# Kernel tuning notes

Measured on AMD Instinct MI355X. Metric: run time of the kernel, lower is better.

Reference implementation:

```python
import jax, jax.numpy as jnp
import numpy as np


def log_g(x):
    # log of g(x) = where(x>=0, x+0.5, sigmoid(x))
    return jnp.where(x >= 0, jnp.log(jax.nn.relu(x) + 0.5), -jax.nn.softplus(-x))


def heinsen_scan_log(log_coeffs, log_values):
    # associative scan in log space over seq dim (axis=1)
    a_star = jnp.cumsum(log_coeffs, axis=1)
    log_h0_plus_b_star = jax.lax.cumlogsumexp(log_values - a_star, axis=1)
    return jnp.exp(a_star + log_h0_plus_b_star)


def setup_inputs() -> dict:
    key = jax.random.key(0)
    k1, k2, k3 = jax.random.split(key, 3)
    B, S, D_IN, D_INNER, D_OUT = 4, 4096, 1024, 1024, 1024
    x = jax.random.normal(k1, (B, S, D_IN), dtype=jnp.float32)
    # xavier_normal for Linear(d_in, 2*d_inner): std = sqrt(2/(fan_in+fan_out))
    std_hg = float(np.sqrt(2.0 / (D_IN + 2 * D_INNER)))
    W_hg = jax.random.normal(k2, (2 * D_INNER, D_IN), dtype=jnp.float32) * std_hg
    std_out = float(np.sqrt(2.0 / (D_INNER + D_OUT)))
    W_out = jax.random.normal(k3, (D_OUT, D_INNER), dtype=jnp.float32) * std_out
    return {"x": x, "W_hg": W_hg, "W_out": W_out}


def reference(x, W_hg, W_out):
    # x: [B,S,Din]; W_hg: [2*Dinner, Din]; W_out: [Dout, Dinner]
    hg = jnp.einsum("bsd,ed->bse", x, W_hg)
    hidden, gate = jnp.split(hg, 2, axis=-1)
    log_coeffs = -jax.nn.softplus(gate)        # log(1 - z)
    log_z = -jax.nn.softplus(-gate)            # log(z)
    log_values = log_z + log_g(hidden)
    h = heinsen_scan_log(log_coeffs, log_values)  # [B,S,Dinner]
    out = jnp.einsum("bsd,od->bso", h, W_out)
    return out
```

## Files before the change

kernel.cpp:

```cpp
#include <hip/hip_runtime.h>
#include <math.h>


typedef unsigned short ushort_t;
typedef unsigned int uint_t;
typedef __attribute__((ext_vector_type(4))) float f32x4;
typedef __attribute__((ext_vector_type(8))) __bf16 bf16x8;
typedef __attribute__((ext_vector_type(8))) unsigned short u16x8;

constexpr int Bsz  = 4;
constexpr int S    = 4096;
constexpr int Din  = 1024;
constexpr int Dh   = 1024;
constexpr int M    = Bsz * S;
constexpr int NCH  = 64;
constexpr int CL   = S / NCH;

__device__ __forceinline__ unsigned short f2bf(float f) {
    unsigned int u = __float_as_uint(f);
    unsigned int r = (u + 0x7fffu + ((u >> 16) & 1u)) >> 16;
    return (unsigned short)r;
}
__device__ __forceinline__ float bf2f(unsigned short u) {
    return __uint_as_float(((unsigned int)u) << 16);
}
__device__ __forceinline__ float sigf(float x) {
    x = fminf(fmaxf(x, -30.f), 30.f);
    return 1.0f / (1.0f + __expf(-x));
}
__device__ __forceinline__ void gld_lds16(const ushort_t* g, ushort_t* l) {
    __builtin_amdgcn_global_load_lds(
        (const __attribute__((address_space(1))) void*)g,
        (__attribute__((address_space(3))) void*)l, 16, 0, 0);
}

__global__ __launch_bounds__(256) void cvt_all(
    const float* __restrict__ x, const float* __restrict__ whg,
    const float* __restrict__ wout,
    ushort_t* __restrict__ xb, ushort_t* __restrict__ whgb,
    ushort_t* __restrict__ woutb)
{
    constexpr int NX = M * Din / 8;
    constexpr int NW = 2048 * 1024 / 8;
    const int i = blockIdx.x * 256 + threadIdx.x;
    const float* src; ushort_t* dst; int k;
    if (i < NX)            { src = x;    dst = xb;    k = i; }
    else if (i < NX + NW)  { src = whg;  dst = whgb;  k = i - NX; }
    else                   { src = wout; dst = woutb; k = i - NX - NW; }
    const float4 a = ((const float4*)src)[(size_t)k * 2];
    const float4 b = ((const float4*)src)[(size_t)k * 2 + 1];
    u16x8 o;
    o[0] = f2bf(a.x); o[1] = f2bf(a.y); o[2] = f2bf(a.z); o[3] = f2bf(a.w);
    o[4] = f2bf(b.x); o[5] = f2bf(b.y); o[6] = f2bf(b.z); o[7] = f2bf(b.w);
    ((u16x8*)dst)[k] = o;
}

template<bool OUT_BF16>
__global__ __launch_bounds__(512, 2) void gemm8p(
    const ushort_t* __restrict__ A, int lda,
    const ushort_t* __restrict__ B, int ldb,
    void* __restrict__ Cout, int ldc, int K, int nbx_log2)
{
    __shared__ ushort_t lds[4][2][8192];

    const int P = K >> 5;

    const int nwg = gridDim.x;
    const int cpx = nwg >> 3;
    const int bid = blockIdx.x;
    const int swz = (bid & 7) * cpx + (bid >> 3);
    const int bx  = swz & ((1 << nbx_log2) - 1);
    const int by  = swz >> nbx_log2;
    const int bm0 = by * 256;
    const int bn0 = bx * 256;

    const int t  = threadIdx.x;
    const int w  = t >> 6;
    const int l  = t & 63;
    const int wr = w >> 2;
    const int wc = w & 3;

    const int fr = l & 15;
    const int kg = l >> 4;
    const int qp = kg ^ (((fr >> 3) & 1) << 1);
    const int a_base = wr * 4096 + fr * 32 + qp * 8;
    const int b_base = wc * 2048 + fr * 32 + qp * 8;

    const int rs = l >> 2;
    const int lq = (l & 3) ^ (((rs >> 3) & 1) << 1);
    const ushort_t* gA0 = A + (size_t)(bm0 + w * 16 + rs) * lda + lq * 8;
    const ushort_t* gA1 = gA0 + (size_t)128 * lda;
    const ushort_t* gB0 = B + (size_t)(bn0 + w * 16 + rs) * ldb + lq * 8;
    const ushort_t* gB1 = gB0 + (size_t)128 * ldb;

    f32x4 acc[8][4];
    #pragma unroll
    for (int i = 0; i < 8; ++i)
        #pragma unroll
        for (int j = 0; j < 4; ++j)
            acc[i][j] = (f32x4){0.f, 0.f, 0.f, 0.f};

    auto stageA = [&](int p) {
        const int s2 = p & 3;
        const int ko = p * 32;
        gld_lds16(gA0 + ko, &lds[s2][0][w * 512]);
        gld_lds16(gA1 + ko, &lds[s2][0][w * 512 + 4096]);
    };
    auto stageB = [&](int p) {
        const int s2 = p & 3;
        const int ko = p * 32;
        gld_lds16(gB0 + ko, &lds[s2][1][w * 512]);
        gld_lds16(gB1 + ko, &lds[s2][1][w * 512 + 4096]);
    };

    stageA(0); stageB(0); stageA(1); stageB(1);
    asm volatile("s_waitcnt vmcnt(4)" ::: "memory");
    __builtin_amdgcn_s_barrier();
    __builtin_amdgcn_sched_barrier(0);

    #pragma unroll 1
    for (int p = 0; p < P; ++p) {
        const int s = p & 3;
        const ushort_t* la = &lds[s][0][0];
        const ushort_t* lb = &lds[s][1][0];
        bf16x8 bfr[4], af0[4], af1[4];

        #pragma unroll
        for (int j = 0; j < 4; ++j)
            bfr[j] = *reinterpret_cast<const bf16x8*>(&lb[b_base + j * 512]);
        #pragma unroll
        for (int i = 0; i < 4; ++i)
            af0[i] = *reinterpret_cast<const bf16x8*>(&la[a_base + i * 512]);
        if (p + 2 < P) stageA(p + 2);
        __builtin_amdgcn_sched_barrier(0);
        __builtin_amdgcn_s_barrier();
        asm volatile("s_waitcnt lgkmcnt(0)" ::: "memory");
        __builtin_amdgcn_sched_barrier(0);
        __builtin_amdgcn_s_setprio(1);
        #pragma unroll
        for (int i = 0; i < 4; ++i)
            #pragma unroll
            for (int j = 0; j < 4; ++j)
                acc[i][j] = __builtin_amdgcn_mfma_f32_16x16x32_bf16(
                    af0[i], bfr[j], acc[i][j], 0, 0, 0);
        __builtin_amdgcn_s_setprio(0);
        __builtin_amdgcn_sched_barrier(0);
        #pragma unroll
        for (int i = 0; i < 4; ++i)
            af1[i] = *reinterpret_cast<const bf16x8*>(&la[a_base + (4 + i) * 512]);
        __builtin_amdgcn_sched_barrier(0);
        __builtin_amdgcn_s_barrier();
        __builtin_amdgcn_sched_barrier(0);

        if (p + 2 < P) stageB(p + 2);
        __builtin_amdgcn_sched_barrier(0);
        if (p + 2 < P)
            asm volatile("s_waitcnt vmcnt(4)" ::: "memory");
        else if (p + 1 < P)
            asm volatile("s_waitcnt vmcnt(0)" ::: "memory");
        __builtin_amdgcn_s_barrier();
        asm volatile("s_waitcnt lgkmcnt(0)" ::: "memory");
        __builtin_amdgcn_sched_barrier(0);
        __builtin_amdgcn_s_setprio(1);
        #pragma unroll
        for (int i = 0; i < 4; ++i)
            #pragma unroll
            for (int j = 0; j < 4; ++j)
                acc[4 + i][j] = __builtin_amdgcn_mfma_f32_16x16x32_bf16(
                    af1[i], bfr[j], acc[4 + i][j], 0, 0, 0);
        __builtin_amdgcn_s_setprio(0);
        __builtin_amdgcn_sched_barrier(0);
        __builtin_amdgcn_s_barrier();
        __builtin_amdgcn_sched_barrier(0);
    }

    #pragma unroll
    for (int i = 0; i < 8; ++i) {
        #pragma unroll
        for (int j = 0; j < 4; ++j) {
            const int col = bn0 + wc * 64 + j * 16 + fr;
            #pragma unroll
            for (int r = 0; r < 4; ++r) {
                const int row = bm0 + wr * 128 + i * 16 + kg * 4 + r;
                if (OUT_BF16)
                    ((ushort_t*)Cout)[(size_t)row * ldc + col] = f2bf(acc[i][j][r]);
                else
                    ((float*)Cout)[(size_t)row * ldc + col] = acc[i][j][r];
            }
        }
    }
}


__global__ __launch_bounds__(256) void scan_stage1(
    const ushort_t* __restrict__ hg, float* __restrict__ Abuf,
    float* __restrict__ hlbuf)
{
    const int bid   = blockIdx.x;
    const int half  = bid & 1;
    const int chunk = (bid >> 1) & (NCH - 1);
    const int b     = bid >> 7;
    const int t     = threadIdx.x;
    const int d     = half * 512 + 2 * t;
    const size_t rowbase = (size_t)(b * S + chunk * CL) * 2048 + d;

    float h0 = 0.f, h1 = 0.f, A0 = 1.f, A1 = 1.f;
    #pragma unroll 4
    for (int i = 0; i < CL; ++i) {
        const ushort_t* rp = hg + rowbase + (size_t)i * 2048;
        const uint_t hp = *(const uint_t*)rp;
        const uint_t gp = *(const uint_t*)(rp + 1024);
        const float hid0 = bf2f((ushort_t)hp), hid1 = bf2f((ushort_t)(hp >> 16));
        const float g0 = bf2f((ushort_t)gp),  g1 = bf2f((ushort_t)(gp >> 16));
        const float c0 = sigf(-g0), z0 = 1.f - c0;
        const float c1 = sigf(-g1), z1 = 1.f - c1;
        const float gv0 = (hid0 >= 0.f) ? (hid0 + 0.5f) : sigf(hid0);
        const float gv1 = (hid1 >= 0.f) ? (hid1 + 0.5f) : sigf(hid1);
        h0 = fmaf(c0, h0, z0 * gv0);  A0 *= c0;
        h1 = fmaf(c1, h1, z1 * gv1);  A1 *= c1;
    }
    const size_t pb = (size_t)(b * NCH + chunk) * 1024 + d;
    *(float2*)&Abuf[pb]  = make_float2(A0, A1);
    *(float2*)&hlbuf[pb] = make_float2(h0, h1);
}

__global__ __launch_bounds__(256) void scan_stage2(
    const float* __restrict__ Abuf, const float* __restrict__ hlbuf,
    float* __restrict__ Hs)
{
    const int g = blockIdx.x * 256 + threadIdx.x;
    const int d = g & (Dh - 1);
    const int b = g >> 10;
    float h = 0.0f;
    for (int ch = 0; ch < NCH; ++ch) {
        const size_t o = (size_t)(b * NCH + ch) * Dh + d;
        Hs[o] = h;
        h = fmaf(Abuf[o], h, hlbuf[o]);
    }
}

__global__ __launch_bounds__(256) void scan_stage3(
    const ushort_t* __restrict__ hg, const float* __restrict__ Hs,
    ushort_t* __restrict__ hout)
{
    const int bid   = blockIdx.x;
    const int half  = bid & 1;
    const int chunk = (bid >> 1) & (NCH - 1);
    const int b     = bid >> 7;
    const int t     = threadIdx.x;
    const int d     = half * 512 + 2 * t;
    const size_t rowbase = (size_t)(b * S + chunk * CL) * 2048 + d;
    const size_t hb      = (size_t)(b * S + chunk * CL) * 1024 + d;

    const float2 hs = *(const float2*)&Hs[(size_t)(b * NCH + chunk) * 1024 + d];
    float h0 = hs.x, h1 = hs.y;
    #pragma unroll 4
    for (int i = 0; i < CL; ++i) {
        const ushort_t* rp = hg + rowbase + (size_t)i * 2048;
        const uint_t hp = *(const uint_t*)rp;
        const uint_t gp = *(const uint_t*)(rp + 1024);
        const float hid0 = bf2f((ushort_t)hp), hid1 = bf2f((ushort_t)(hp >> 16));
        const float g0 = bf2f((ushort_t)gp),  g1 = bf2f((ushort_t)(gp >> 16));
        const float c0 = sigf(-g0), z0 = 1.f - c0;
        const float c1 = sigf(-g1), z1 = 1.f - c1;
        const float gv0 = (hid0 >= 0.f) ? (hid0 + 0.5f) : sigf(hid0);
        const float gv1 = (hid1 >= 0.f) ? (hid1 + 0.5f) : sigf(hid1);
        h0 = fmaf(c0, h0, z0 * gv0);
        h1 = fmaf(c1, h1, z1 * gv1);
        const uint_t o = (uint_t)f2bf(h0) | ((uint_t)f2bf(h1) << 16);
        *(uint_t*)(hout + hb + (size_t)i * 1024) = o;
    }
}

extern "C" void kernel_launch(void* const* d_in, const int* in_sizes, int n_in,
                              void* d_out, int out_size, void* d_ws, size_t ws_size,
                              hipStream_t stream)
{
    (void)in_sizes; (void)n_in; (void)out_size; (void)ws_size;
    const float* x    = (const float*)d_in[0];
    const float* Whg  = (const float*)d_in[1];
    const float* Wout = (const float*)d_in[2];
    float* out = (float*)d_out;

    ushort_t* hgbuf = (ushort_t*)d_ws;
    ushort_t* xb    = hgbuf + (size_t)M * 2048;
    ushort_t* whgb  = xb + (size_t)M * 1024;
    ushort_t* woutb = whgb + (size_t)2048 * 1024;
    float*    Abuf  = (float*)(woutb + (size_t)1024 * 1024);
    float*    hlbuf = Abuf + (size_t)Bsz * NCH * Dh;
    float*    Hsbuf = hlbuf + (size_t)Bsz * NCH * Dh;

    const dim3 blk(256);

    cvt_all<<<dim3(9728), blk, 0, stream>>>(x, Whg, Wout, xb, whgb, woutb);

    gemm8p<true><<<dim3(512), dim3(512), 0, stream>>>(
        xb, Din, whgb, Din, hgbuf, 2048, Din, 3);

    scan_stage1<<<dim3(512), blk, 0, stream>>>(hgbuf, Abuf, hlbuf);
    scan_stage2<<<dim3(Bsz * Dh / 256), blk, 0, stream>>>(Abuf, hlbuf, Hsbuf);
    scan_stage3<<<dim3(512), blk, 0, stream>>>(hgbuf, Hsbuf, xb);

    gemm8p<false><<<dim3(256), dim3(512), 0, stream>>>(
        xb, Dh, woutb, Din, out, 1024, Dh, 2);
}
```

Measured before the change: 209.8 us.

## Use 4-wave GEMM with 128x128 per-wave tiles and single-phase pipeline

Replaces the 8-wave 256x256 GEMM with a 4-wave version where each wave computes a 128x128 sub-tile (8x8 MFMA accumulators), which doubles register reuse of the A and B fragments. The two half-phase split with its extra barriers is collapsed into a single barrier per K step, and all A and B loads for a stage are issued together. This lowers LDS reads per MFMA and cuts synchronisation. In exchange each wave needs about 256 accumulator registers, so only one block fits per CU, and there are fewer waves left to hide latency.

```diff
diff --git a/kernel.cpp b/kernel.cpp
--- a/kernel.cpp
+++ b/kernel.cpp
@@ -56,7 +56,7 @@
 }
 
 template<bool OUT_BF16>
-__global__ __launch_bounds__(512, 2) void gemm8p(
+__global__ __launch_bounds__(256, 1) void gemmfat(
     const ushort_t* __restrict__ A, int lda,
     const ushort_t* __restrict__ B, int ldb,
     void* __restrict__ Cout, int ldc, int K, int nbx_log2)
@@ -77,108 +77,80 @@
     const int t  = threadIdx.x;
     const int w  = t >> 6;
     const int l  = t & 63;
-    const int wr = w >> 2;
-    const int wc = w & 3;
+    const int wr = w >> 1;
+    const int wc = w & 1;
 
     const int fr = l & 15;
     const int kg = l >> 4;
     const int qp = kg ^ (((fr >> 3) & 1) << 1);
     const int a_base = wr * 4096 + fr * 32 + qp * 8;
-    const int b_base = wc * 2048 + fr * 32 + qp * 8;
+    const int b_base = wc * 4096 + fr * 32 + qp * 8;
 
     const int rs = l >> 2;
     const int lq = (l & 3) ^ (((rs >> 3) & 1) << 1);
     const ushort_t* gA0 = A + (size_t)(bm0 + w * 16 + rs) * lda + lq * 8;
-    const ushort_t* gA1 = gA0 + (size_t)128 * lda;
     const ushort_t* gB0 = B + (size_t)(bn0 + w * 16 + rs) * ldb + lq * 8;
-    const ushort_t* gB1 = gB0 + (size_t)128 * ldb;
-
-    f32x4 acc[8][4];
+    const size_t a64 = (size_t)64 * lda;
+    const size_t b64 = (size_t)64 * ldb;
+
+    f32x4 acc[8][8];
     #pragma unroll
     for (int i = 0; i < 8; ++i)
         #pragma unroll
-        for (int j = 0; j < 4; ++j)
+        for (int j = 0; j < 8; ++j)
             acc[i][j] = (f32x4){0.f, 0.f, 0.f, 0.f};
 
-    auto stageA = [&](int p) {
+    auto stage = [&](int p) {
         const int s2 = p & 3;
         const int ko = p * 32;
-        gld_lds16(gA0 + ko, &lds[s2][0][w * 512]);
-        gld_lds16(gA1 + ko, &lds[s2][0][w * 512 + 4096]);
+        #pragma unroll
+        for (int q = 0; q < 4; ++q) {
+            gld_lds16(gA0 + (size_t)q * a64 + ko, &lds[s2][0][w * 512 + q * 2048]);
+            gld_lds16(gB0 + (size_t)q * b64 + ko, &lds[s2][1][w * 512 + q * 2048]);
+        }
     };
-    auto stageB = [&](int p) {
-        const int s2 = p & 3;
-        const int ko = p * 32;
-        gld_lds16(gB0 + ko, &lds[s2][1][w * 512]);
-        gld_lds16(gB1 + ko, &lds[s2][1][w * 512 + 4096]);
-    };
-
-    stageA(0); stageB(0); stageA(1); stageB(1);
-    asm volatile("s_waitcnt vmcnt(4)" ::: "memory");
-    __builtin_amdgcn_s_barrier();
-    __builtin_amdgcn_sched_barrier(0);
-
-    #pragma unroll 1
-    for (int p = 0; p < P; ++p) {
+
+    auto phase_body = [&](int p, bool do_stage) {
+        __builtin_amdgcn_s_barrier();
+        __builtin_amdgcn_sched_barrier(0);
         const int s = p & 3;
         const ushort_t* la = &lds[s][0][0];
         const ushort_t* lb = &lds[s][1][0];
-        bf16x8 bfr[4], af0[4], af1[4];
-
-        #pragma unroll
-        for (int j = 0; j < 4; ++j)
+        bf16x8 af[8], bfr[8];
+        #pragma unroll
+        for (int i = 0; i < 8; ++i)
+            af[i] = *reinterpret_cast<const bf16x8*>(&la[a_base + i * 512]);
+        #pragma unroll
+        for (int j = 0; j < 8; ++j)
             bfr[j] = *reinterpret_cast<const bf16x8*>(&lb[b_base + j * 512]);
-        #pragma unroll
-        for (int i = 0; i < 4; ++i)
-            af0[i] = *reinterpret_cast<const bf16x8*>(&la[a_base + i * 512]);
-        if (p + 2 < P) stageA(p + 2);
-        __builtin_amdgcn_sched_barrier(0);
-        __builtin_amdgcn_s_barrier();
-        asm volatile("s_waitcnt lgkmcnt(0)" ::: "memory");
+        if (do_stage) stage(p + 2);
         __builtin_amdgcn_sched_barrier(0);
         __builtin_amdgcn_s_setprio(1);
         #pragma unroll
-        for (int i = 0; i < 4; ++i)
+        for (int i = 0; i < 8; ++i)
             #pragma unroll
-            for (int j = 0; j < 4; ++j)
+            for (int j = 0; j < 8; ++j)
                 acc[i][j] = __builtin_amdgcn_mfma_f32_16x16x32_bf16(
-                    af0[i], bfr[j], acc[i][j], 0, 0, 0);
+                    af[i], bfr[j], acc[i][j], 0, 0, 0);
         __builtin_amdgcn_s_setprio(0);
         __builtin_amdgcn_sched_barrier(0);
-        #pragma unroll
-        for (int i = 0; i < 4; ++i)
-            af1[i] = *reinterpret_cast<const bf16x8*>(&la[a_base + (4 + i) * 512]);
-        __builtin_amdgcn_sched_barrier(0);
-        __builtin_amdgcn_s_barrier();
-        __builtin_amdgcn_sched_barrier(0);
-
-        if (p + 2 < P) stageB(p + 2);
-        __builtin_amdgcn_sched_barrier(0);
-        if (p + 2 < P)
-            asm volatile("s_waitcnt vmcnt(4)" ::: "memory");
-        else if (p + 1 < P)
-            asm volatile("s_waitcnt vmcnt(0)" ::: "memory");
-        __builtin_amdgcn_s_barrier();
-        asm volatile("s_waitcnt lgkmcnt(0)" ::: "memory");
-        __builtin_amdgcn_sched_barrier(0);
-        __builtin_amdgcn_s_setprio(1);
-        #pragma unroll
-        for (int i = 0; i < 4; ++i)
-            #pragma unroll
-            for (int j = 0; j < 4; ++j)
-                acc[4 + i][j] = __builtin_amdgcn_mfma_f32_16x16x32_bf16(
-                    af1[i], bfr[j], acc[4 + i][j], 0, 0, 0);
-        __builtin_amdgcn_s_setprio(0);
-        __builtin_amdgcn_sched_barrier(0);
-        __builtin_amdgcn_s_barrier();
-        __builtin_amdgcn_sched_barrier(0);
-    }
+    };
+
+    stage(0);
+    stage(1);
+
+    for (int p = 0; p < P - 1; ++p) {
+        asm volatile("s_waitcnt vmcnt(8)" ::: "memory");
+        phase_body(p, p < P - 2);
+    }
+    asm volatile("s_waitcnt vmcnt(0)" ::: "memory");
+    phase_body(P - 1, false);
 
     #pragma unroll
     for (int i = 0; i < 8; ++i) {
         #pragma unroll
-        for (int j = 0; j < 4; ++j) {
-            const int col = bn0 + wc * 64 + j * 16 + fr;
+        for (int j = 0; j < 8; ++j) {
+            const int col = bn0 + wc * 128 + j * 16 + fr;
             #pragma unroll
             for (int r = 0; r < 4; ++r) {
                 const int row = bm0 + wr * 128 + i * 16 + kg * 4 + r;
@@ -294,13 +266,13 @@
 
     cvt_all<<<dim3(9728), blk, 0, stream>>>(x, Whg, Wout, xb, whgb, woutb);
 
-    gemm8p<true><<<dim3(512), dim3(512), 0, stream>>>(
+    gemmfat<true><<<dim3(512), blk, 0, stream>>>(
         xb, Din, whgb, Din, hgbuf, 2048, Din, 3);
 
     scan_stage1<<<dim3(512), blk, 0, stream>>>(hgbuf, Abuf, hlbuf);
     scan_stage2<<<dim3(Bsz * Dh / 256), blk, 0, stream>>>(Abuf, hlbuf, Hsbuf);
     scan_stage3<<<dim3(512), blk, 0, stream>>>(hgbuf, Hsbuf, xb);
 
-    gemm8p<false><<<dim3(256), dim3(512), 0, stream>>>(
+    gemmfat<false><<<dim3(256), blk, 0, stream>>>(
         xb, Dh, woutb, Din, out, 1024, Dh, 2);
 }
```

New measurement: 210.3 us. About the same (+0.2%).

## Load GEMM B fragments directly from global into registers, halving LDS staging

Applied to the files above, without the earlier changes.

The GEMM no longer stages the B (weight) tile through LDS. Each wave instead loads its B fragments straight from global memory into double-buffered registers one k-step ahead, and only the A tile is staged into LDS. The loop is restructured into one barrier per k-step with all 8 A fragments read at once, which removes a barrier and halves LDS traffic and footprint. In exchange, B reads are no longer shared across the waves in a row, so global/L2 traffic for B rises, and the per-thread strided global loads may coalesce poorly.

```diff
diff --git a/kernel.cpp b/kernel.cpp
--- a/kernel.cpp
+++ b/kernel.cpp
@@ -56,12 +56,12 @@
 }
 
 template<bool OUT_BF16>
-__global__ __launch_bounds__(512, 2) void gemm8p(
+__global__ __launch_bounds__(512, 2) void gemm_breg(
     const ushort_t* __restrict__ A, int lda,
     const ushort_t* __restrict__ B, int ldb,
     void* __restrict__ Cout, int ldc, int K, int nbx_log2)
 {
-    __shared__ ushort_t lds[4][2][8192];
+    __shared__ ushort_t lds[4][8192];
 
     const int P = K >> 5;
 
@@ -84,14 +84,16 @@
     const int kg = l >> 4;
     const int qp = kg ^ (((fr >> 3) & 1) << 1);
     const int a_base = wr * 4096 + fr * 32 + qp * 8;
-    const int b_base = wc * 2048 + fr * 32 + qp * 8;
 
     const int rs = l >> 2;
     const int lq = (l & 3) ^ (((rs >> 3) & 1) << 1);
     const ushort_t* gA0 = A + (size_t)(bm0 + w * 16 + rs) * lda + lq * 8;
     const ushort_t* gA1 = gA0 + (size_t)128 * lda;
-    const ushort_t* gB0 = B + (size_t)(bn0 + w * 16 + rs) * ldb + lq * 8;
-    const ushort_t* gB1 = gB0 + (size_t)128 * ldb;
+
+    const ushort_t* gB[4];
+    #pragma unroll
+    for (int j = 0; j < 4; ++j)
+        gB[j] = B + (size_t)(bn0 + wc * 64 + j * 16 + fr) * ldb + kg * 8;
 
     f32x4 acc[8][4];
     #pragma unroll
@@ -103,75 +105,59 @@
     auto stageA = [&](int p) {
         const int s2 = p & 3;
         const int ko = p * 32;
-        gld_lds16(gA0 + ko, &lds[s2][0][w * 512]);
-        gld_lds16(gA1 + ko, &lds[s2][0][w * 512 + 4096]);
+        gld_lds16(gA0 + ko, &lds[s2][w * 512]);
+        gld_lds16(gA1 + ko, &lds[s2][w * 512 + 4096]);
     };
-    auto stageB = [&](int p) {
-        const int s2 = p & 3;
-        const int ko = p * 32;
-        gld_lds16(gB0 + ko, &lds[s2][1][w * 512]);
-        gld_lds16(gB1 + ko, &lds[s2][1][w * 512 + 4096]);
-    };
-
-    stageA(0); stageB(0); stageA(1); stageB(1);
-    asm volatile("s_waitcnt vmcnt(4)" ::: "memory");
+
+    bf16x8 bfrA[4], bfrB[4];
+
+    #pragma unroll
+    for (int j = 0; j < 4; ++j)
+        bfrA[j] = *(const bf16x8*)(gB[j]);
+    stageA(0);
+    stageA(1);
+    __builtin_amdgcn_sched_barrier(0);
+    asm volatile("s_waitcnt vmcnt(2)" ::: "memory");
     __builtin_amdgcn_s_barrier();
     __builtin_amdgcn_sched_barrier(0);
 
-    #pragma unroll 1
-    for (int p = 0; p < P; ++p) {
-        const int s = p & 3;
-        const ushort_t* la = &lds[s][0][0];
-        const ushort_t* lb = &lds[s][1][0];
-        bf16x8 bfr[4], af0[4], af1[4];
-
-        #pragma unroll
-        for (int j = 0; j < 4; ++j)
-            bfr[j] = *reinterpret_cast<const bf16x8*>(&lb[b_base + j * 512]);
-        #pragma unroll
-        for (int i = 0; i < 4; ++i)
-            af0[i] = *reinterpret_cast<const bf16x8*>(&la[a_base + i * 512]);
+    auto phase = [&](int p, bf16x8 (&cur)[4], bf16x8 (&nxt)[4]) {
+        const ushort_t* la = &lds[p & 3][0];
+        bf16x8 af[8];
+        #pragma unroll
+        for (int i = 0; i < 8; ++i)
+            af[i] = *reinterpret_cast<const bf16x8*>(&la[a_base + i * 512]);
+        if (p + 1 < P) {
+            #pragma unroll
+            for (int j = 0; j < 4; ++j)
+                nxt[j] = *(const bf16x8*)(gB[j] + (p + 1) * 32);
+        }
         if (p + 2 < P) stageA(p + 2);
         __builtin_amdgcn_sched_barrier(0);
-        __builtin_amdgcn_s_barrier();
+        if (p < P - 2)
+            asm volatile("s_waitcnt vmcnt(6)" ::: "memory");
+        else if (p == P - 2)
+            asm volatile("s_waitcnt vmcnt(4)" ::: "memory");
+        else
+            asm volatile("s_waitcnt vmcnt(0)" ::: "memory");
         asm volatile("s_waitcnt lgkmcnt(0)" ::: "memory");
         __builtin_amdgcn_sched_barrier(0);
         __builtin_amdgcn_s_setprio(1);
         #pragma unroll
-        for (int i = 0; i < 4; ++i)
+        for (int i = 0; i < 8; ++i)
             #pragma unroll
             for (int j = 0; j < 4; ++j)
                 acc[i][j] = __builtin_amdgcn_mfma_f32_16x16x32_bf16(
-                    af0[i], bfr[j], acc[i][j], 0, 0, 0);
-        __builtin_amdgcn_s_setprio(0);
-        __builtin_amdgcn_sched_barrier(0);
-        #pragma unroll
-        for (int i = 0; i < 4; ++i)
-            af1[i] = *reinterpret_cast<const bf16x8*>(&la[a_base + (4 + i) * 512]);
-        __builtin_amdgcn_sched_barrier(0);
-        __builtin_amdgcn_s_barrier();
-        __builtin_amdgcn_sched_barrier(0);
-
-        if (p + 2 < P) stageB(p + 2);
-        __builtin_amdgcn_sched_barrier(0);
-        if (p + 2 < P)
-            asm volatile("s_waitcnt vmcnt(4)" ::: "memory");
-        else if (p + 1 < P)
-            asm volatile("s_waitcnt vmcnt(0)" ::: "memory");
-        __builtin_amdgcn_s_barrier();
-        asm volatile("s_waitcnt lgkmcnt(0)" ::: "memory");
-        __builtin_amdgcn_sched_barrier(0);
-        __builtin_amdgcn_s_setprio(1);
-        #pragma unroll
-        for (int i = 0; i < 4; ++i)
-            #pragma unroll
-            for (int j = 0; j < 4; ++j)
-                acc[4 + i][j] = __builtin_amdgcn_mfma_f32_16x16x32_bf16(
-                    af1[i], bfr[j], acc[4 + i][j], 0, 0, 0);
+                    af[i], cur[j], acc[i][j], 0, 0, 0);
         __builtin_amdgcn_s_setprio(0);
         __builtin_amdgcn_sched_barrier(0);
         __builtin_amdgcn_s_barrier();
-        __builtin_amdgcn_sched_barrier(0);
+    };
+
+    #pragma unroll 1
+    for (int p = 0; p < P; p += 2) {
+        phase(p,     bfrA, bfrB);
+        phase(p + 1, bfrB, bfrA);
     }
 
     #pragma unroll
@@ -294,13 +280,13 @@
 
     cvt_all<<<dim3(9728), blk, 0, stream>>>(x, Whg, Wout, xb, whgb, woutb);
 
-    gemm8p<true><<<dim3(512), dim3(512), 0, stream>>>(
+    gemm_breg<true><<<dim3(512), dim3(512), 0, stream>>>(
         xb, Din, whgb, Din, hgbuf, 2048, Din, 3);
 
     scan_stage1<<<dim3(512), blk, 0, stream>>>(hgbuf, Abuf, hlbuf);
     scan_stage2<<<dim3(Bsz * Dh / 256), blk, 0, stream>>>(Abuf, hlbuf, Hsbuf);
     scan_stage3<<<dim3(512), blk, 0, stream>>>(hgbuf, Hsbuf, xb);
 
-    gemm8p<false><<<dim3(256), dim3(512), 0, stream>>>(
+    gemm_breg<false><<<dim3(256), dim3(512), 0, stream>>>(
         xb, Dh, woutb, Din, out, 1024, Dh, 2);
 }
```

Result: slower. 251.7 us (+20.0%).
